# Kernel tuning notes

Hardware: AMD Instinct MI355X
Metric: run time of the kernel (lower is better)

## Reference

```python
import jax, jax.numpy as jnp
import numpy as np

N = 100000
C_IN = 128
HEADS = 4
D_HEAD = 32
E = 1600000
NEG_SLOPE = 0.2
LN_EPS = 1e-5


def setup_inputs() -> dict:
    key = jax.random.key(0)
    ks = jax.random.split(key, 8)
    x = jax.random.normal(ks[0], (N, C_IN), dtype=jnp.float32)
    edge_index = jax.random.randint(ks[1], (2, E), 0, N, dtype=jnp.int32)
    # LayerNorm affine params
    ln_gamma = jnp.ones((C_IN,), jnp.float32)
    ln_beta = jnp.zeros((C_IN,), jnp.float32)
    # GATv2 linear layers (lin_l for source/messages, lin_r for target), glorot-ish scale
    scale = 1.0 / np.sqrt(C_IN)
    W_l = jax.random.normal(ks[2], (C_IN, HEADS * D_HEAD), jnp.float32) * scale
    b_l = jnp.zeros((HEADS * D_HEAD,), jnp.float32)
    W_r = jax.random.normal(ks[3], (C_IN, HEADS * D_HEAD), jnp.float32) * scale
    b_r = jnp.zeros((HEADS * D_HEAD,), jnp.float32)
    att = jax.random.normal(ks[4], (HEADS, D_HEAD), jnp.float32) * (1.0 / np.sqrt(D_HEAD))
    bias = jnp.zeros((D_HEAD,), jnp.float32)  # concat=False -> out_channels bias
    return {"x": x, "edge_index": edge_index, "ln_gamma": ln_gamma, "ln_beta": ln_beta,
            "W_l": W_l, "b_l": b_l, "W_r": W_r, "b_r": b_r, "att": att, "bias": bias}


def reference(x, edge_index, ln_gamma, ln_beta, W_l, b_l, W_r, b_r, att, bias):
    n = x.shape[0]
    # LayerNorm + ReLU (dropout_mask=None / eval mode)
    mu = jnp.mean(x, axis=-1, keepdims=True)
    var = jnp.mean(jnp.square(x - mu), axis=-1, keepdims=True)
    xh = (x - mu) * jax.lax.rsqrt(var + LN_EPS) * ln_gamma + ln_beta
    xh = jax.nn.relu(xh)
    # add self loops
    loops = jnp.arange(n, dtype=edge_index.dtype)
    src = jnp.concatenate([edge_index[0], loops])  # message sources j
    dst = jnp.concatenate([edge_index[1], loops])  # aggregation targets i
    # GATv2: separate transforms for source and target
    x_l = (xh @ W_l + b_l).reshape(n, HEADS, D_HEAD)
    x_r = (xh @ W_r + b_r).reshape(n, HEADS, D_HEAD)
    # edge scores: e_ij = att . leaky_relu(x_l[j] + x_r[i])
    s = x_l[src] + x_r[dst]                                      # [E+N, H, Dh]
    e = jnp.einsum('ehd,hd->eh', jax.nn.leaky_relu(s, NEG_SLOPE), att)
    # segment softmax over destination node
    m = jax.ops.segment_max(e, dst, num_segments=n)              # [N, H]
    w = jnp.exp(e - m[dst])
    denom = jax.ops.segment_sum(w, dst, num_segments=n)          # [N, H]
    alpha = w / (denom[dst] + 1e-16)                             # [E+N, H]
    # scatter-aggregate messages alpha * x_l[j]
    out = jax.ops.segment_sum(alpha[:, :, None] * x_l[src], dst, num_segments=n)  # [N, H, Dh]
    # concat=False -> mean over heads, then bias
    return out.mean(axis=1) + bias
```

## Files before the change

kernel.cpp:

```cpp
#include <hip/hip_runtime.h>
#include <math.h>


typedef __bf16 bf16x8 __attribute__((ext_vector_type(8)));
typedef float f32x4 __attribute__((ext_vector_type(4)));
typedef _Float16 h2 __attribute__((ext_vector_type(2)));

#define BIN_T 4096
#define NB_MAX 1024
#define AST 136
#define HST 136

static __device__ __forceinline__ unsigned short f2bf(float f) {
  union { float f; unsigned u; } v;
  v.f = f;
  const unsigned r = v.u + 0x7fffu + ((v.u >> 16) & 1u);
  return (unsigned short)(r >> 16);
}
static __device__ __forceinline__ float bf2f(unsigned short h) {
  union { float f; unsigned u; } v;
  v.u = ((unsigned)h) << 16;
  return v.f;
}

static __device__ __forceinline__ float quad_reduce_add(float p) {
  int a = __builtin_amdgcn_mov_dpp(__builtin_bit_cast(int, p),
                                   0xB1 , 0xf, 0xf,
                                   true);
  p += __builtin_bit_cast(float, a);
  int b = __builtin_amdgcn_mov_dpp(__builtin_bit_cast(int, p),
                                   0x4E , 0xf, 0xf,
                                   true);
  p += __builtin_bit_cast(float, b);
  return p;
}

__global__ __launch_bounds__(256) void pack_w_k(
    const float* __restrict__ Wl, const float* __restrict__ Wr,
    unsigned short* __restrict__ wph, unsigned short* __restrict__ wpl) {
  const int idx = blockIdx.x * 256 + threadIdx.x;
  const int mat = idx >> 14;
  const int rem = idx & 16383;
  const int k = rem >> 7;
  const int c = rem & 127;
  const float v = (mat ? Wr : Wl)[rem];
  const unsigned short h = f2bf(v);
  const unsigned short lo = f2bf(v - bf2f(h));
  const int po = ((mat * 4 + (k >> 5)) * 128 + c) * 32 + (k & 31);
  wph[po] = h;
  wpl[po] = lo;
}

__global__ __launch_bounds__(512, 5) void ln_gemm_mfma_k(
    const float* __restrict__ x, const float* __restrict__ gamma,
    const float* __restrict__ beta,
    const unsigned short* __restrict__ wph,
    const unsigned short* __restrict__ wpl,
    const float* __restrict__ bl, const float* __restrict__ br,
    _Float16* __restrict__ xl16, _Float16* __restrict__ xr16, int n) {
  __shared__ char smem[64 * AST * 2 * 2];
  unsigned short* const ah = (unsigned short*)smem;
  unsigned short* const al = ah + 64 * AST;
  _Float16* const sth = (_Float16*)smem;

  const int t = threadIdx.x;
  const int blk = blockIdx.x * 64;

  {
    const int r = t >> 3, q = t & 7;
    const int node = blk + r;
    float4 v[4];
    float s = 0.f, s2 = 0.f;
    const float* xrow = x + (size_t)node * 128;
#pragma unroll
    for (int rep = 0; rep < 4; rep++) {
      float4 f = make_float4(0.f, 0.f, 0.f, 0.f);
      if (node < n) f = *(const float4*)(xrow + 4 * q + 32 * rep);
      v[rep] = f;
      s += f.x + f.y + f.z + f.w;
      s2 += f.x * f.x + f.y * f.y + f.z * f.z + f.w * f.w;
    }
    s += __shfl_xor(s, 1);  s += __shfl_xor(s, 2);  s += __shfl_xor(s, 4);
    s2 += __shfl_xor(s2, 1); s2 += __shfl_xor(s2, 2); s2 += __shfl_xor(s2, 4);
    const float mu = s * (1.f / 128.f);
    const float rs = rsqrtf(s2 * (1.f / 128.f) - mu * mu + 1e-5f);
#pragma unroll
    for (int rep = 0; rep < 4; rep++) {
      const int k0 = 4 * q + 32 * rep;
      const float4 g4 = *(const float4*)(gamma + k0);
      const float4 b4 = *(const float4*)(beta + k0);
      const float ev[4] = {v[rep].x, v[rep].y, v[rep].z, v[rep].w};
      const float gv[4] = {g4.x, g4.y, g4.z, g4.w};
      const float bv[4] = {b4.x, b4.y, b4.z, b4.w};
      unsigned short hs[4], ls[4];
#pragma unroll
      for (int i2 = 0; i2 < 4; i2++) {
        float xv = (ev[i2] - mu) * rs * gv[i2] + bv[i2];
        xv = fmaxf(xv, 0.f);
        const unsigned short h = f2bf(xv);
        hs[i2] = h;
        ls[i2] = f2bf(xv - bf2f(h));
      }
      *(ushort4*)(&ah[r * AST + k0]) = make_ushort4(hs[0], hs[1], hs[2], hs[3]);
      *(ushort4*)(&al[r * AST + k0]) = make_ushort4(ls[0], ls[1], ls[2], ls[3]);
    }
  }
  __syncthreads();

  const int lane = t & 63;
  const int w = t >> 6;
  const int mat = w >> 2;
  const int cbase = (w & 3) * 32;
  const int m16 = lane & 15;
  const int quad = lane >> 4;
  const float* const biasp = mat ? br : bl;

  f32x4 acc[2][4];
  float bc[2];
#pragma unroll
  for (int ct = 0; ct < 2; ct++) {
    const int c = cbase + ct * 16 + m16;
    bf16x8 Bh[4], Bl8[4];
#pragma unroll
    for (int kb = 0; kb < 4; kb++) {
      const int bo = ((mat * 4 + kb) * 128 + c) * 32 + quad * 8;
      Bh[kb]  = *(const bf16x8*)(wph + bo);
      Bl8[kb] = *(const bf16x8*)(wpl + bo);
    }
    bc[ct] = biasp[c];
#pragma unroll
    for (int rt = 0; rt < 4; rt++) {
      f32x4 a = {0.f, 0.f, 0.f, 0.f};
#pragma unroll
      for (int kb = 0; kb < 4; kb++) {
        const int ao = (rt * 16 + m16) * AST + kb * 32 + quad * 8;
        const bf16x8 Ah  = *(const bf16x8*)(ah + ao);
        const bf16x8 Al8 = *(const bf16x8*)(al + ao);
        a = __builtin_amdgcn_mfma_f32_16x16x32_bf16(Ah,  Bh[kb],  a, 0, 0, 0);
        a = __builtin_amdgcn_mfma_f32_16x16x32_bf16(Al8, Bh[kb],  a, 0, 0, 0);
        a = __builtin_amdgcn_mfma_f32_16x16x32_bf16(Ah,  Bl8[kb], a, 0, 0, 0);
      }
      acc[ct][rt] = a;
    }
  }

  unsigned short* const outs[2] = {(unsigned short*)xl16,
                                   (unsigned short*)xr16};
#pragma unroll
  for (int round = 0; round < 2; round++) {
    __syncthreads();
    if (mat == 1 - round) {
#pragma unroll
      for (int ct = 0; ct < 2; ct++)
#pragma unroll
        for (int rt = 0; rt < 4; rt++)
#pragma unroll
          for (int g = 0; g < 4; g++)
            sth[(rt * 16 + quad * 4 + g) * HST + cbase + ct * 16 + m16] =
                (_Float16)(acc[ct][rt][g] + bc[ct]);
    }
    __syncthreads();
    unsigned short* const dst = outs[1 - round];
#pragma unroll
    for (int pass = 0; pass < 2; pass++) {
      const int idx = pass * 512 + t;
      const int row = idx >> 4;
      const int c8 = (idx & 15) * 8;
      const int node = blk + row;
      if (node < n)
        *(uint4*)(dst + (size_t)node * 128 + c8) =
            *(const uint4*)((const unsigned short*)sth + row * HST + c8);
    }
  }
}

__global__ __launch_bounds__(256) void hist_lds_k(
    const int* __restrict__ dst_arr, int* __restrict__ bucket_cnt,
    int E, int NB) {
  __shared__ int h[NB_MAX];
  const int t = threadIdx.x;
  for (int b = t; b < NB; b += 256) h[b] = 0;
  __syncthreads();
  const int beg = blockIdx.x * BIN_T;
  const int end = min(beg + BIN_T, E);
  for (int j0 = beg + t * 4; j0 < end; j0 += 1024) {
    if (j0 + 4 <= end) {
      const int4 d4 = *(const int4*)(dst_arr + j0);
      atomicAdd(&h[d4.x >> 7], 1);
      atomicAdd(&h[d4.y >> 7], 1);
      atomicAdd(&h[d4.z >> 7], 1);
      atomicAdd(&h[d4.w >> 7], 1);
    } else {
      for (int j = j0; j < end; j++) atomicAdd(&h[dst_arr[j] >> 7], 1);
    }
  }
  __syncthreads();
  for (int b = t; b < NB; b += 256) {
    const int v = h[b];
    if (v) atomicAdd(&bucket_cnt[b], v);
  }
}

__global__ __launch_bounds__(1024) void bucket_scan_k(
    const int* __restrict__ bucket_cnt, int* __restrict__ bucket_edge_off,
    int* __restrict__ bucket_cur, int* __restrict__ offsets,
    int NB, int N, int M) {
  __shared__ int lds[1024];
  const int t = threadIdx.x;
  const int v = (t < NB) ? bucket_cnt[t] : 0;
  lds[t] = v;
  __syncthreads();
  for (int d = 1; d < 1024; d <<= 1) {
    int u = 0;
    if (t >= d) u = lds[t - d];
    __syncthreads();
    lds[t] += u;
    __syncthreads();
  }
  if (t < NB) {
    const int excl = lds[t] - v;
    bucket_edge_off[t] = excl;
    bucket_cur[t] = excl;
    if (t == NB - 1) bucket_edge_off[NB] = lds[t];
  }
  if (t == 0) offsets[N] = M;
}

__global__ __launch_bounds__(256) void bin2_k(
    const int* __restrict__ ei, int* __restrict__ bucket_cur,
    unsigned* __restrict__ binned, int E, int NB) {
  __shared__ int h[NB_MAX];
  __shared__ int cur[NB_MAX];
  const int t = threadIdx.x;
  for (int b = t; b < NB; b += 256) h[b] = 0;
  __syncthreads();
  const int beg = blockIdx.x * BIN_T;
  const int end = min(beg + BIN_T, E);
  for (int j0 = beg + t * 4; j0 < end; j0 += 1024) {
    if (j0 + 4 <= end) {
      const int4 d4 = *(const int4*)(ei + E + j0);
      atomicAdd(&h[d4.x >> 7], 1);
      atomicAdd(&h[d4.y >> 7], 1);
      atomicAdd(&h[d4.z >> 7], 1);
      atomicAdd(&h[d4.w >> 7], 1);
    } else {
      for (int j = j0; j < end; j++) atomicAdd(&h[ei[E + j] >> 7], 1);
    }
  }
  __syncthreads();
  for (int b = t; b < NB; b += 256) {
    const int v = h[b];
    cur[b] = v ? atomicAdd(&bucket_cur[b], v) : 0;
  }
  __syncthreads();
  for (int j0 = beg + t * 4; j0 < end; j0 += 1024) {
    if (j0 + 4 <= end) {
      const int4 s4 = *(const int4*)(ei + j0);
      const int4 d4 = *(const int4*)(ei + E + j0);
      binned[atomicAdd(&cur[d4.x >> 7], 1)] =
          (((unsigned)d4.x & 127u) << 25) | (unsigned)s4.x;
      binned[atomicAdd(&cur[d4.y >> 7], 1)] =
          (((unsigned)d4.y & 127u) << 25) | (unsigned)s4.y;
      binned[atomicAdd(&cur[d4.z >> 7], 1)] =
          (((unsigned)d4.z & 127u) << 25) | (unsigned)s4.z;
      binned[atomicAdd(&cur[d4.w >> 7], 1)] =
          (((unsigned)d4.w & 127u) << 25) | (unsigned)s4.w;
    } else {
      for (int j = j0; j < end; j++) {
        const int s = ei[j], d = ei[E + j];
        binned[atomicAdd(&cur[d >> 7], 1)] =
            (((unsigned)d & 127u) << 25) | (unsigned)s;
      }
    }
  }
}

__global__ __launch_bounds__(256) void csr_build_k(
    const unsigned* __restrict__ binned,
    const int* __restrict__ bucket_edge_off,
    unsigned* __restrict__ csr_src, int* __restrict__ offsets, int N, int M) {
  __shared__ int s_cnt[128];
  __shared__ int s_off[128];
  __shared__ int s_cur[128];
  const int b = blockIdx.x;
  const int t = threadIdx.x;
  if (b == 0 && t < 16) csr_src[M + t] = 0;
  const int eb = bucket_edge_off[b];
  const int ee = bucket_edge_off[b + 1];
  const int node0 = b << 7;
  if (t < 128) s_cnt[t] = 0;
  __syncthreads();
  for (int j = eb + t; j < ee; j += 256) {
    atomicAdd(&s_cnt[binned[j] >> 25], 1);
  }
  __syncthreads();
  int w = 0;
  if (t < 128) w = (node0 + t < N) ? (s_cnt[t] + 1) : 0;
  if (t < 128) s_off[t] = w;
  __syncthreads();
  for (int d = 1; d < 128; d <<= 1) {
    int u = 0;
    if (t < 128 && t >= d) u = s_off[t - d];
    __syncthreads();
    if (t < 128) s_off[t] += u;
    __syncthreads();
  }
  const int base = eb + node0;
  if (t < 128) {
    const int excl = s_off[t] - w;
    const int node = node0 + t;
    if (node < N) {
      offsets[node] = base + excl;
      csr_src[base + excl] = (unsigned)node << 8;
      s_cur[t] = excl + 1;
    }
  }
  __syncthreads();
  for (int j = eb + t; j < ee; j += 256) {
    const unsigned e = binned[j];
    const int pos = atomicAdd(&s_cur[e >> 25], 1);
    csr_src[base + pos] = (e & 0x1ffffffu) << 8;
  }
}

__global__ __launch_bounds__(256) void agg_fused_k(
    const uint4* __restrict__ xl4, const uint4* __restrict__ xr4,
    const float* __restrict__ att, const unsigned* __restrict__ csr_src,
    const int* __restrict__ offsets, const float* __restrict__ bias,
    float* __restrict__ out, int n) {
  const int t = threadIdx.x;
  const int wid = t >> 6;
  const int lane = t & 63;
  const int u = lane & 15;
  const int g = lane >> 4;
  const int nwaves = gridDim.x * 4;

  h2 at[4];
  {
    const float L2E = 1.44269504f;
    const float4 a0 = *(const float4*)(att + u * 8);
    const float4 a1 = *(const float4*)(att + u * 8 + 4);
    at[0] = h2{(_Float16)(a0.x * L2E), (_Float16)(a0.y * L2E)};
    at[1] = h2{(_Float16)(a0.z * L2E), (_Float16)(a0.w * L2E)};
    at[2] = h2{(_Float16)(a1.x * L2E), (_Float16)(a1.y * L2E)};
    at[3] = h2{(_Float16)(a1.z * L2E), (_Float16)(a1.w * L2E)};
  }
  float4 b0, b1;
  if (lane < 4) {
    b0 = *(const float4*)(bias + lane * 8);
    b1 = *(const float4*)(bias + lane * 8 + 4);
  }

  const h2 slope = h2{(_Float16)0.2f, (_Float16)0.2f};
  const char* const xbu = (const char*)xl4 + ((unsigned)u << 4);
  union U { uint4 u4; h2 h[4]; unsigned ui[4]; };

  int i = blockIdx.x * 4 + wid;
  if (i >= n) return;

  int off = offsets[i];
  int end = offsets[i + 1];
  U xru; xru.u4 = xr4[(size_t)i * 16 + u];
  uint4 rA = *(const uint4*)(xbu + csr_src[off + g]);
  uint4 rB = *(const uint4*)(xbu + csr_src[off + 4 + g]);

  while (true) {
    const int inext = i + nwaves;
    const int isel = (inext < n) ? inext : i;
    const int offn = offsets[isel];
    const int endn = offsets[isel + 1];
    U xrn; xrn.u4 = xr4[(size_t)isel * 16 + u];

    float den = 0.f;
    float acc[8] = {0.f, 0.f, 0.f, 0.f, 0.f, 0.f, 0.f, 0.f};

    for (int jb = off; jb < end; jb += 4) {
      U xv; xv.u4 = rA;
      rA = rB;
      rB = *(const uint4*)(xbu + csr_src[jb + 8 + g]);

      float p = 0.f;
#pragma unroll
      for (int k = 0; k < 4; k++) {
        const h2 s = xv.h[k] + xru.h[k];
        const h2 l = __builtin_elementwise_max(s, s * slope);
        p = __builtin_amdgcn_fdot2(l, at[k], p, false);
      }
      p = quad_reduce_add(p);

      const float wgt = (jb + g < end) ? __builtin_amdgcn_exp2f(p) : 0.f;
      den += wgt;
#pragma unroll
      for (int k = 0; k < 4; k++) {
        asm("v_fma_mix_f32 %0, %1, %2, %0 op_sel:[0,0,0] op_sel_hi:[0,1,0]"
            : "+v"(acc[2 * k]) : "v"(wgt), "v"(xv.ui[k]));
        asm("v_fma_mix_f32 %0, %1, %2, %0 op_sel:[0,1,0] op_sel_hi:[0,1,0]"
            : "+v"(acc[2 * k + 1]) : "v"(wgt), "v"(xv.ui[k]));
      }
    }

    const unsigned niA = csr_src[offn + g];
    const unsigned niB = csr_src[offn + 4 + g];

    den += __shfl_xor(den, 16);
    den += __shfl_xor(den, 32);
#pragma unroll
    for (int m = 0; m < 8; m++) {
      acc[m] += __shfl_xor(acc[m], 16);
      acc[m] += __shfl_xor(acc[m], 32);
    }
    const float rd = 1.0f / (den + 1e-16f);
#pragma unroll
    for (int m = 0; m < 8; m++) acc[m] *= rd;
#pragma unroll
    for (int m = 0; m < 8; m++) {
      acc[m] += __shfl_xor(acc[m], 4);
      acc[m] += __shfl_xor(acc[m], 8);
    }
    if (lane < 4) {
      float4 o0 = make_float4(acc[0] * 0.25f + b0.x, acc[1] * 0.25f + b0.y,
                              acc[2] * 0.25f + b0.z, acc[3] * 0.25f + b0.w);
      float4 o1 = make_float4(acc[4] * 0.25f + b1.x, acc[5] * 0.25f + b1.y,
                              acc[6] * 0.25f + b1.z, acc[7] * 0.25f + b1.w);
      *(float4*)(out + (size_t)i * 32 + lane * 8) = o0;
      *(float4*)(out + (size_t)i * 32 + lane * 8 + 4) = o1;
    }

    if (inext >= n) break;
    i = inext;
    off = offn;
    end = endn;
    xru = xrn;
    rA = *(const uint4*)(xbu + niA);
    rB = *(const uint4*)(xbu + niB);
  }
}

extern "C" void kernel_launch(void* const* d_in, const int* in_sizes, int n_in,
                              void* d_out, int out_size, void* d_ws,
                              size_t ws_size, hipStream_t stream) {
  const float* x     = (const float*)d_in[0];
  const int*   ei    = (const int*)d_in[1];
  const float* gamma = (const float*)d_in[2];
  const float* beta  = (const float*)d_in[3];
  const float* Wl    = (const float*)d_in[4];
  const float* bl    = (const float*)d_in[5];
  const float* Wr    = (const float*)d_in[6];
  const float* br    = (const float*)d_in[7];
  const float* att   = (const float*)d_in[8];
  const float* bias  = (const float*)d_in[9];
  float* out = (float*)d_out;

  const int N = in_sizes[0] / 128;
  const int E = in_sizes[1] / 2;
  const int M = E + N;
  const int NB = (N + 127) / 128;
  const int nchunks = (E + BIN_T - 1) / BIN_T;

  char* p = (char*)d_ws;
  size_t o = 0;
  auto alloc = [&](size_t bytes) -> void* {
    void* r = (void*)(p + o);
    o = (o + bytes + 255) & ~(size_t)255;
    return r;
  };
  _Float16* xl16   = (_Float16*)alloc((size_t)N * 128 * 2);
  unsigned* binned = (unsigned*)xl16;
  _Float16* xr16 = (_Float16*)alloc((size_t)N * 128 * 2);
  unsigned* csr_src = (unsigned*)alloc((size_t)M * 4 + 64);
  int*   offsets = (int*)alloc((size_t)(N + 1) * 4);
  int*   bucket_cnt = (int*)alloc((size_t)NB * 4);
  int*   bucket_off = (int*)alloc((size_t)(NB + 1) * 4);
  int*   bucket_cur = (int*)alloc((size_t)NB * 4);
  unsigned short* wph = (unsigned short*)alloc(2 * 128 * 128 * 2);
  unsigned short* wpl = (unsigned short*)alloc(2 * 128 * 128 * 2);
  (void)n_in; (void)out_size; (void)ws_size;

  hipMemsetAsync(bucket_cnt, 0, (size_t)NB * 4, stream);
  hist_lds_k<<<nchunks, 256, 0, stream>>>(ei + E, bucket_cnt, E, NB);
  bucket_scan_k<<<1, 1024, 0, stream>>>(bucket_cnt, bucket_off, bucket_cur,
                                        offsets, NB, N, M);
  bin2_k<<<nchunks, 256, 0, stream>>>(ei, bucket_cur, binned, E, NB);
  csr_build_k<<<NB, 256, 0, stream>>>(binned, bucket_off, csr_src, offsets,
                                      N, M);

  pack_w_k<<<128, 256, 0, stream>>>(Wl, Wr, wph, wpl);
  ln_gemm_mfma_k<<<(N + 63) / 64, 512, 0, stream>>>(x, gamma, beta, wph, wpl,
                                                    bl, br, xl16, xr16, N);

  const int nodeWaves = (N + 3) / 4;
  const int aggBlocks = nodeWaves < 2048 ? nodeWaves : 2048;
  agg_fused_k<<<aggBlocks, 256, 0, stream>>>((const uint4*)xl16,
                                             (const uint4*)xr16, att,
                                             csr_src, offsets, bias, out, N);
}
```

Before: 257.6 us.

## Fold bucket scan and weight packing into neighboring kernels to cut launches

Removes the separate bucket_scan and pack_w kernels. The weight bf16 split-packing moves into the histogram kernel, and each bin2/csr_build block recomputes the bucket prefix scan from the raw counts. bin2 now starts from a zeroed per-bucket cursor plus the scanned offset. BIN_T is doubled, which halves the block count for histogram and binning. Two fewer launches and their serialization gaps are traded for a redundant scan in every block and fewer, larger binning blocks.

```diff
diff --git a/kernel.cpp b/kernel.cpp
--- a/kernel.cpp
+++ b/kernel.cpp
@@ -6,7 +6,7 @@
 typedef float f32x4 __attribute__((ext_vector_type(4)));
 typedef _Float16 h2 __attribute__((ext_vector_type(2)));
 
-#define BIN_T 4096
+#define BIN_T 8192
 #define NB_MAX 1024
 #define AST 136
 #define HST 136
@@ -33,22 +33,6 @@
                                    true);
   p += __builtin_bit_cast(float, b);
   return p;
-}
-
-__global__ __launch_bounds__(256) void pack_w_k(
-    const float* __restrict__ Wl, const float* __restrict__ Wr,
-    unsigned short* __restrict__ wph, unsigned short* __restrict__ wpl) {
-  const int idx = blockIdx.x * 256 + threadIdx.x;
-  const int mat = idx >> 14;
-  const int rem = idx & 16383;
-  const int k = rem >> 7;
-  const int c = rem & 127;
-  const float v = (mat ? Wr : Wl)[rem];
-  const unsigned short h = f2bf(v);
-  const unsigned short lo = f2bf(v - bf2f(h));
-  const int po = ((mat * 4 + (k >> 5)) * 128 + c) * 32 + (k & 31);
-  wph[po] = h;
-  wpl[po] = lo;
 }
 
 __global__ __launch_bounds__(512, 5) void ln_gemm_mfma_k(
@@ -174,12 +158,27 @@
   }
 }
 
-__global__ __launch_bounds__(256) void hist_lds_k(
+__global__ __launch_bounds__(256) void hist_pack_k(
     const int* __restrict__ dst_arr, int* __restrict__ bucket_cnt,
+    const float* __restrict__ Wl, const float* __restrict__ Wr,
+    unsigned short* __restrict__ wph, unsigned short* __restrict__ wpl,
     int E, int NB) {
   __shared__ int h[NB_MAX];
   const int t = threadIdx.x;
+  const int gtid = blockIdx.x * 256 + t;
   for (int b = t; b < NB; b += 256) h[b] = 0;
+  if (gtid < 32768) {
+    const int mat = gtid >> 14;
+    const int rem = gtid & 16383;
+    const int k = rem >> 7;
+    const int c = rem & 127;
+    const float v = (mat ? Wr : Wl)[rem];
+    const unsigned short hh = f2bf(v);
+    const unsigned short lo = f2bf(v - bf2f(hh));
+    const int po = ((mat * 4 + (k >> 5)) * 128 + c) * 32 + (k & 31);
+    wph[po] = hh;
+    wpl[po] = lo;
+  }
   __syncthreads();
   const int beg = blockIdx.x * BIN_T;
   const int end = min(beg + BIN_T, E);
@@ -201,36 +200,13 @@
   }
 }
 
-__global__ __launch_bounds__(1024) void bucket_scan_k(
-    const int* __restrict__ bucket_cnt, int* __restrict__ bucket_edge_off,
-    int* __restrict__ bucket_cur, int* __restrict__ offsets,
-    int NB, int N, int M) {
-  __shared__ int lds[1024];
-  const int t = threadIdx.x;
-  const int v = (t < NB) ? bucket_cnt[t] : 0;
-  lds[t] = v;
-  __syncthreads();
-  for (int d = 1; d < 1024; d <<= 1) {
-    int u = 0;
-    if (t >= d) u = lds[t - d];
-    __syncthreads();
-    lds[t] += u;
-    __syncthreads();
-  }
-  if (t < NB) {
-    const int excl = lds[t] - v;
-    bucket_edge_off[t] = excl;
-    bucket_cur[t] = excl;
-    if (t == NB - 1) bucket_edge_off[NB] = lds[t];
-  }
-  if (t == 0) offsets[N] = M;
-}
-
 __global__ __launch_bounds__(256) void bin2_k(
-    const int* __restrict__ ei, int* __restrict__ bucket_cur,
-    unsigned* __restrict__ binned, int E, int NB) {
+    const int* __restrict__ ei, const int* __restrict__ bucket_cnt,
+    int* __restrict__ bucket_cur, unsigned* __restrict__ binned,
+    int E, int NB) {
   __shared__ int h[NB_MAX];
   __shared__ int cur[NB_MAX];
+  __shared__ int ld2[256];
   const int t = threadIdx.x;
   for (int b = t; b < NB; b += 256) h[b] = 0;
   __syncthreads();
@@ -248,9 +224,32 @@
     }
   }
   __syncthreads();
-  for (int b = t; b < NB; b += 256) {
-    const int v = h[b];
-    cur[b] = v ? atomicAdd(&bucket_cur[b], v) : 0;
+  {
+    int pre[4], gsum = 0;
+#pragma unroll
+    for (int k = 0; k < 4; k++) {
+      const int idx = t * 4 + k;
+      const int v = (idx < NB) ? bucket_cnt[idx] : 0;
+      pre[k] = gsum;
+      gsum += v;
+    }
+    ld2[t] = gsum;
+    __syncthreads();
+    for (int d = 1; d < 256; d <<= 1) {
+      int uv = (t >= d) ? ld2[t - d] : 0;
+      __syncthreads();
+      ld2[t] += uv;
+      __syncthreads();
+    }
+    const int ex = (t > 0) ? ld2[t - 1] : 0;
+#pragma unroll
+    for (int k = 0; k < 4; k++) {
+      const int idx = t * 4 + k;
+      if (idx < NB) {
+        const int v = h[idx];
+        cur[idx] = ex + pre[k] + (v ? atomicAdd(&bucket_cur[idx], v) : 0);
+      }
+    }
   }
   __syncthreads();
   for (int j0 = beg + t * 4; j0 < end; j0 += 1024) {
@@ -276,20 +275,47 @@
 }
 
 __global__ __launch_bounds__(256) void csr_build_k(
-    const unsigned* __restrict__ binned,
-    const int* __restrict__ bucket_edge_off,
-    unsigned* __restrict__ csr_src, int* __restrict__ offsets, int N, int M) {
+    const unsigned* __restrict__ binned, const int* __restrict__ bucket_cnt,
+    unsigned* __restrict__ csr_src, int* __restrict__ offsets,
+    int N, int M, int NB) {
   __shared__ int s_cnt[128];
   __shared__ int s_off[128];
   __shared__ int s_cur[128];
+  __shared__ int ld2[256];
+  __shared__ int s_eb;
   const int b = blockIdx.x;
   const int t = threadIdx.x;
   if (b == 0 && t < 16) csr_src[M + t] = 0;
-  const int eb = bucket_edge_off[b];
-  const int ee = bucket_edge_off[b + 1];
+  if (b == 0 && t == 0) offsets[N] = M;
+  {
+    int pre[4], gsum = 0;
+#pragma unroll
+    for (int k = 0; k < 4; k++) {
+      const int idx = t * 4 + k;
+      const int v = (idx < NB) ? bucket_cnt[idx] : 0;
+      pre[k] = gsum;
+      gsum += v;
+    }
+    ld2[t] = gsum;
+    __syncthreads();
+    for (int d = 1; d < 256; d <<= 1) {
+      int uv = (t >= d) ? ld2[t - d] : 0;
+      __syncthreads();
+      ld2[t] += uv;
+      __syncthreads();
+    }
+    const int ex = (t > 0) ? ld2[t - 1] : 0;
+#pragma unroll
+    for (int k = 0; k < 4; k++) {
+      const int idx = t * 4 + k;
+      if (idx == b) s_eb = ex + pre[k];
+    }
+  }
+  if (t < 128) s_cnt[t] = 0;
+  __syncthreads();
+  const int eb = s_eb;
+  const int ee = eb + bucket_cnt[b];
   const int node0 = b << 7;
-  if (t < 128) s_cnt[t] = 0;
-  __syncthreads();
   for (int j = eb + t; j < ee; j += 256) {
     atomicAdd(&s_cnt[binned[j] >> 25], 1);
   }
@@ -469,22 +495,23 @@
   _Float16* xr16 = (_Float16*)alloc((size_t)N * 128 * 2);
   unsigned* csr_src = (unsigned*)alloc((size_t)M * 4 + 64);
   int*   offsets = (int*)alloc((size_t)(N + 1) * 4);
-  int*   bucket_cnt = (int*)alloc((size_t)NB * 4);
-  int*   bucket_off = (int*)alloc((size_t)(NB + 1) * 4);
-  int*   bucket_cur = (int*)alloc((size_t)NB * 4);
+  int*   bucket_cnt = (int*)alloc((size_t)NB * 2 * 4);
+  int*   bucket_cur = bucket_cnt + NB;
   unsigned short* wph = (unsigned short*)alloc(2 * 128 * 128 * 2);
   unsigned short* wpl = (unsigned short*)alloc(2 * 128 * 128 * 2);
   (void)n_in; (void)out_size; (void)ws_size;
 
-  hipMemsetAsync(bucket_cnt, 0, (size_t)NB * 4, stream);
-  hist_lds_k<<<nchunks, 256, 0, stream>>>(ei + E, bucket_cnt, E, NB);
-  bucket_scan_k<<<1, 1024, 0, stream>>>(bucket_cnt, bucket_off, bucket_cur,
-                                        offsets, NB, N, M);
-  bin2_k<<<nchunks, 256, 0, stream>>>(ei, bucket_cur, binned, E, NB);
-  csr_build_k<<<NB, 256, 0, stream>>>(binned, bucket_off, csr_src, offsets,
-                                      N, M);
-
-  pack_w_k<<<128, 256, 0, stream>>>(Wl, Wr, wph, wpl);
+  hipMemsetAsync(bucket_cnt, 0, (size_t)NB * 2 * 4, stream);
+  {
+    const int grid = nchunks > 128 ? nchunks : 128;
+    hist_pack_k<<<grid, 256, 0, stream>>>(ei + E, bucket_cnt, Wl, Wr, wph,
+                                          wpl, E, NB);
+  }
+  bin2_k<<<nchunks, 256, 0, stream>>>(ei, bucket_cnt, bucket_cur, binned,
+                                      E, NB);
+  csr_build_k<<<NB, 256, 0, stream>>>(binned, bucket_cnt, csr_src, offsets,
+                                      N, M, NB);
+
   ln_gemm_mfma_k<<<(N + 63) / 64, 512, 0, stream>>>(x, gamma, beta, wph, wpl,
                                                     bl, br, xl16, xr16, N);
 
```

Result: slower. 269.2 us (+4.5%).

## Merge weight packing into histogram and co-schedule binning with LN-GEMM blocks

Applied to the files above, without the earlier changes.

Folds the weight bf16 hi/lo packing into the histogram kernel, so the first edge-index pass also does the packing. The edge binning pass and the LayerNorm+MFMA GEMM now run in one launch, with the first nchunks blocks binning edges and the rest computing xl/xr. Because xl16 is now written at the same time as binning, the binned scratch moves into the output buffer, which csr_build consumes before the aggregation kernel overwrites it. This removes two launches and lets the memory-bound scatter overlap the compute-heavy GEMM. In exchange the binning blocks now run with 512 threads, capped by the GEMM's launch bounds.

```diff
diff --git a/kernel.cpp b/kernel.cpp
--- a/kernel.cpp
+++ b/kernel.cpp
@@ -35,151 +35,27 @@
   return p;
 }
 
-__global__ __launch_bounds__(256) void pack_w_k(
+__global__ __launch_bounds__(256) void hist_pack_k(
+    const int* __restrict__ dst_arr, int* __restrict__ bucket_cnt,
     const float* __restrict__ Wl, const float* __restrict__ Wr,
-    unsigned short* __restrict__ wph, unsigned short* __restrict__ wpl) {
-  const int idx = blockIdx.x * 256 + threadIdx.x;
-  const int mat = idx >> 14;
-  const int rem = idx & 16383;
-  const int k = rem >> 7;
-  const int c = rem & 127;
-  const float v = (mat ? Wr : Wl)[rem];
-  const unsigned short h = f2bf(v);
-  const unsigned short lo = f2bf(v - bf2f(h));
-  const int po = ((mat * 4 + (k >> 5)) * 128 + c) * 32 + (k & 31);
-  wph[po] = h;
-  wpl[po] = lo;
-}
-
-__global__ __launch_bounds__(512, 5) void ln_gemm_mfma_k(
-    const float* __restrict__ x, const float* __restrict__ gamma,
-    const float* __restrict__ beta,
-    const unsigned short* __restrict__ wph,
-    const unsigned short* __restrict__ wpl,
-    const float* __restrict__ bl, const float* __restrict__ br,
-    _Float16* __restrict__ xl16, _Float16* __restrict__ xr16, int n) {
-  __shared__ char smem[64 * AST * 2 * 2];
-  unsigned short* const ah = (unsigned short*)smem;
-  unsigned short* const al = ah + 64 * AST;
-  _Float16* const sth = (_Float16*)smem;
-
-  const int t = threadIdx.x;
-  const int blk = blockIdx.x * 64;
-
-  {
-    const int r = t >> 3, q = t & 7;
-    const int node = blk + r;
-    float4 v[4];
-    float s = 0.f, s2 = 0.f;
-    const float* xrow = x + (size_t)node * 128;
-#pragma unroll
-    for (int rep = 0; rep < 4; rep++) {
-      float4 f = make_float4(0.f, 0.f, 0.f, 0.f);
-      if (node < n) f = *(const float4*)(xrow + 4 * q + 32 * rep);
-      v[rep] = f;
-      s += f.x + f.y + f.z + f.w;
-      s2 += f.x * f.x + f.y * f.y + f.z * f.z + f.w * f.w;
-    }
-    s += __shfl_xor(s, 1);  s += __shfl_xor(s, 2);  s += __shfl_xor(s, 4);
-    s2 += __shfl_xor(s2, 1); s2 += __shfl_xor(s2, 2); s2 += __shfl_xor(s2, 4);
-    const float mu = s * (1.f / 128.f);
-    const float rs = rsqrtf(s2 * (1.f / 128.f) - mu * mu + 1e-5f);
-#pragma unroll
-    for (int rep = 0; rep < 4; rep++) {
-      const int k0 = 4 * q + 32 * rep;
-      const float4 g4 = *(const float4*)(gamma + k0);
-      const float4 b4 = *(const float4*)(beta + k0);
-      const float ev[4] = {v[rep].x, v[rep].y, v[rep].z, v[rep].w};
-      const float gv[4] = {g4.x, g4.y, g4.z, g4.w};
-      const float bv[4] = {b4.x, b4.y, b4.z, b4.w};
-      unsigned short hs[4], ls[4];
-#pragma unroll
-      for (int i2 = 0; i2 < 4; i2++) {
-        float xv = (ev[i2] - mu) * rs * gv[i2] + bv[i2];
-        xv = fmaxf(xv, 0.f);
-        const unsigned short h = f2bf(xv);
-        hs[i2] = h;
-        ls[i2] = f2bf(xv - bf2f(h));
-      }
-      *(ushort4*)(&ah[r * AST + k0]) = make_ushort4(hs[0], hs[1], hs[2], hs[3]);
-      *(ushort4*)(&al[r * AST + k0]) = make_ushort4(ls[0], ls[1], ls[2], ls[3]);
-    }
-  }
-  __syncthreads();
-
-  const int lane = t & 63;
-  const int w = t >> 6;
-  const int mat = w >> 2;
-  const int cbase = (w & 3) * 32;
-  const int m16 = lane & 15;
-  const int quad = lane >> 4;
-  const float* const biasp = mat ? br : bl;
-
-  f32x4 acc[2][4];
-  float bc[2];
-#pragma unroll
-  for (int ct = 0; ct < 2; ct++) {
-    const int c = cbase + ct * 16 + m16;
-    bf16x8 Bh[4], Bl8[4];
-#pragma unroll
-    for (int kb = 0; kb < 4; kb++) {
-      const int bo = ((mat * 4 + kb) * 128 + c) * 32 + quad * 8;
-      Bh[kb]  = *(const bf16x8*)(wph + bo);
-      Bl8[kb] = *(const bf16x8*)(wpl + bo);
-    }
-    bc[ct] = biasp[c];
-#pragma unroll
-    for (int rt = 0; rt < 4; rt++) {
-      f32x4 a = {0.f, 0.f, 0.f, 0.f};
-#pragma unroll
-      for (int kb = 0; kb < 4; kb++) {
-        const int ao = (rt * 16 + m16) * AST + kb * 32 + quad * 8;
-        const bf16x8 Ah  = *(const bf16x8*)(ah + ao);
-        const bf16x8 Al8 = *(const bf16x8*)(al + ao);
-        a = __builtin_amdgcn_mfma_f32_16x16x32_bf16(Ah,  Bh[kb],  a, 0, 0, 0);
-        a = __builtin_amdgcn_mfma_f32_16x16x32_bf16(Al8, Bh[kb],  a, 0, 0, 0);
-        a = __builtin_amdgcn_mfma_f32_16x16x32_bf16(Ah,  Bl8[kb], a, 0, 0, 0);
-      }
-      acc[ct][rt] = a;
-    }
-  }
-
-  unsigned short* const outs[2] = {(unsigned short*)xl16,
-                                   (unsigned short*)xr16};
-#pragma unroll
-  for (int round = 0; round < 2; round++) {
-    __syncthreads();
-    if (mat == 1 - round) {
-#pragma unroll
-      for (int ct = 0; ct < 2; ct++)
-#pragma unroll
-        for (int rt = 0; rt < 4; rt++)
-#pragma unroll
-          for (int g = 0; g < 4; g++)
-            sth[(rt * 16 + quad * 4 + g) * HST + cbase + ct * 16 + m16] =
-                (_Float16)(acc[ct][rt][g] + bc[ct]);
-    }
-    __syncthreads();
-    unsigned short* const dst = outs[1 - round];
-#pragma unroll
-    for (int pass = 0; pass < 2; pass++) {
-      const int idx = pass * 512 + t;
-      const int row = idx >> 4;
-      const int c8 = (idx & 15) * 8;
-      const int node = blk + row;
-      if (node < n)
-        *(uint4*)(dst + (size_t)node * 128 + c8) =
-            *(const uint4*)((const unsigned short*)sth + row * HST + c8);
-    }
-  }
-}
-
-__global__ __launch_bounds__(256) void hist_lds_k(
-    const int* __restrict__ dst_arr, int* __restrict__ bucket_cnt,
+    unsigned short* __restrict__ wph, unsigned short* __restrict__ wpl,
     int E, int NB) {
   __shared__ int h[NB_MAX];
   const int t = threadIdx.x;
+  const int gtid = blockIdx.x * 256 + t;
   for (int b = t; b < NB; b += 256) h[b] = 0;
+  if (gtid < 32768) {
+    const int mat = gtid >> 14;
+    const int rem = gtid & 16383;
+    const int k = rem >> 7;
+    const int c = rem & 127;
+    const float v = (mat ? Wr : Wl)[rem];
+    const unsigned short hh = f2bf(v);
+    const unsigned short lo = f2bf(v - bf2f(hh));
+    const int po = ((mat * 4 + (k >> 5)) * 128 + c) * 32 + (k & 31);
+    wph[po] = hh;
+    wpl[po] = lo;
+  }
   __syncthreads();
   const int beg = blockIdx.x * BIN_T;
   const int end = min(beg + BIN_T, E);
@@ -226,51 +102,175 @@
   if (t == 0) offsets[N] = M;
 }
 
-__global__ __launch_bounds__(256) void bin2_k(
+__global__ __launch_bounds__(512, 5) void gemm_bin_fat_k(
+    const float* __restrict__ x, const float* __restrict__ gamma,
+    const float* __restrict__ beta,
+    const unsigned short* __restrict__ wph,
+    const unsigned short* __restrict__ wpl,
+    const float* __restrict__ bl, const float* __restrict__ br,
+    _Float16* __restrict__ xl16, _Float16* __restrict__ xr16,
     const int* __restrict__ ei, int* __restrict__ bucket_cur,
-    unsigned* __restrict__ binned, int E, int NB) {
-  __shared__ int h[NB_MAX];
-  __shared__ int cur[NB_MAX];
+    unsigned* __restrict__ binned,
+    int n, int E, int NB, int nchunks) {
+  __shared__ char smem[64 * AST * 2 * 2];
   const int t = threadIdx.x;
-  for (int b = t; b < NB; b += 256) h[b] = 0;
-  __syncthreads();
-  const int beg = blockIdx.x * BIN_T;
-  const int end = min(beg + BIN_T, E);
-  for (int j0 = beg + t * 4; j0 < end; j0 += 1024) {
-    if (j0 + 4 <= end) {
-      const int4 d4 = *(const int4*)(ei + E + j0);
-      atomicAdd(&h[d4.x >> 7], 1);
-      atomicAdd(&h[d4.y >> 7], 1);
-      atomicAdd(&h[d4.z >> 7], 1);
-      atomicAdd(&h[d4.w >> 7], 1);
-    } else {
-      for (int j = j0; j < end; j++) atomicAdd(&h[ei[E + j] >> 7], 1);
-    }
-  }
-  __syncthreads();
-  for (int b = t; b < NB; b += 256) {
-    const int v = h[b];
-    cur[b] = v ? atomicAdd(&bucket_cur[b], v) : 0;
-  }
-  __syncthreads();
-  for (int j0 = beg + t * 4; j0 < end; j0 += 1024) {
-    if (j0 + 4 <= end) {
-      const int4 s4 = *(const int4*)(ei + j0);
-      const int4 d4 = *(const int4*)(ei + E + j0);
-      binned[atomicAdd(&cur[d4.x >> 7], 1)] =
-          (((unsigned)d4.x & 127u) << 25) | (unsigned)s4.x;
-      binned[atomicAdd(&cur[d4.y >> 7], 1)] =
-          (((unsigned)d4.y & 127u) << 25) | (unsigned)s4.y;
-      binned[atomicAdd(&cur[d4.z >> 7], 1)] =
-          (((unsigned)d4.z & 127u) << 25) | (unsigned)s4.z;
-      binned[atomicAdd(&cur[d4.w >> 7], 1)] =
-          (((unsigned)d4.w & 127u) << 25) | (unsigned)s4.w;
-    } else {
-      for (int j = j0; j < end; j++) {
-        const int s = ei[j], d = ei[E + j];
-        binned[atomicAdd(&cur[d >> 7], 1)] =
-            (((unsigned)d & 127u) << 25) | (unsigned)s;
+
+  if ((int)blockIdx.x < nchunks) {
+    int* const h = (int*)smem;
+    int* const cur = h + NB_MAX;
+    for (int b = t; b < NB; b += 512) h[b] = 0;
+    __syncthreads();
+    const int beg = blockIdx.x * BIN_T;
+    const int end = min(beg + BIN_T, E);
+    for (int j0 = beg + t * 4; j0 < end; j0 += 2048) {
+      if (j0 + 4 <= end) {
+        const int4 d4 = *(const int4*)(ei + E + j0);
+        atomicAdd(&h[d4.x >> 7], 1);
+        atomicAdd(&h[d4.y >> 7], 1);
+        atomicAdd(&h[d4.z >> 7], 1);
+        atomicAdd(&h[d4.w >> 7], 1);
+      } else {
+        for (int j = j0; j < end; j++) atomicAdd(&h[ei[E + j] >> 7], 1);
       }
+    }
+    __syncthreads();
+    for (int b = t; b < NB; b += 512) {
+      const int v = h[b];
+      cur[b] = v ? atomicAdd(&bucket_cur[b], v) : 0;
+    }
+    __syncthreads();
+    for (int j0 = beg + t * 4; j0 < end; j0 += 2048) {
+      if (j0 + 4 <= end) {
+        const int4 s4 = *(const int4*)(ei + j0);
+        const int4 d4 = *(const int4*)(ei + E + j0);
+        binned[atomicAdd(&cur[d4.x >> 7], 1)] =
+            (((unsigned)d4.x & 127u) << 25) | (unsigned)s4.x;
+        binned[atomicAdd(&cur[d4.y >> 7], 1)] =
+            (((unsigned)d4.y & 127u) << 25) | (unsigned)s4.y;
+        binned[atomicAdd(&cur[d4.z >> 7], 1)] =
+            (((unsigned)d4.z & 127u) << 25) | (unsigned)s4.z;
+        binned[atomicAdd(&cur[d4.w >> 7], 1)] =
+            (((unsigned)d4.w & 127u) << 25) | (unsigned)s4.w;
+      } else {
+        for (int j = j0; j < end; j++) {
+          const int s = ei[j], d = ei[E + j];
+          binned[atomicAdd(&cur[d >> 7], 1)] =
+              (((unsigned)d & 127u) << 25) | (unsigned)s;
+        }
+      }
+    }
+    return;
+  }
+
+  unsigned short* const ah = (unsigned short*)smem;
+  unsigned short* const al = ah + 64 * AST;
+  _Float16* const sth = (_Float16*)smem;
+  const int blk = (blockIdx.x - nchunks) * 64;
+
+  {
+    const int r = t >> 3, q = t & 7;
+    const int node = blk + r;
+    float4 v[4];
+    float s = 0.f, s2 = 0.f;
+    const float* xrow = x + (size_t)node * 128;
+#pragma unroll
+    for (int rep = 0; rep < 4; rep++) {
+      float4 f = make_float4(0.f, 0.f, 0.f, 0.f);
+      if (node < n) f = *(const float4*)(xrow + 4 * q + 32 * rep);
+      v[rep] = f;
+      s += f.x + f.y + f.z + f.w;
+      s2 += f.x * f.x + f.y * f.y + f.z * f.z + f.w * f.w;
+    }
+    s += __shfl_xor(s, 1);  s += __shfl_xor(s, 2);  s += __shfl_xor(s, 4);
+    s2 += __shfl_xor(s2, 1); s2 += __shfl_xor(s2, 2); s2 += __shfl_xor(s2, 4);
+    const float mu = s * (1.f / 128.f);
+    const float rs = rsqrtf(s2 * (1.f / 128.f) - mu * mu + 1e-5f);
+#pragma unroll
+    for (int rep = 0; rep < 4; rep++) {
+      const int k0 = 4 * q + 32 * rep;
+      const float4 g4 = *(const float4*)(gamma + k0);
+      const float4 b4 = *(const float4*)(beta + k0);
+      const float ev[4] = {v[rep].x, v[rep].y, v[rep].z, v[rep].w};
+      const float gv[4] = {g4.x, g4.y, g4.z, g4.w};
+      const float bv[4] = {b4.x, b4.y, b4.z, b4.w};
+      unsigned short hs[4], ls[4];
+#pragma unroll
+      for (int i2 = 0; i2 < 4; i2++) {
+        float xv = (ev[i2] - mu) * rs * gv[i2] + bv[i2];
+        xv = fmaxf(xv, 0.f);
+        const unsigned short h = f2bf(xv);
+        hs[i2] = h;
+        ls[i2] = f2bf(xv - bf2f(h));
+      }
+      *(ushort4*)(&ah[r * AST + k0]) = make_ushort4(hs[0], hs[1], hs[2], hs[3]);
+      *(ushort4*)(&al[r * AST + k0]) = make_ushort4(ls[0], ls[1], ls[2], ls[3]);
+    }
+  }
+  __syncthreads();
+
+  const int lane = t & 63;
+  const int w = t >> 6;
+  const int mat = w >> 2;
+  const int cbase = (w & 3) * 32;
+  const int m16 = lane & 15;
+  const int quad = lane >> 4;
+  const float* const biasp = mat ? br : bl;
+
+  f32x4 acc[2][4];
+  float bc[2];
+#pragma unroll
+  for (int ct = 0; ct < 2; ct++) {
+    const int c = cbase + ct * 16 + m16;
+    bf16x8 Bh[4], Bl8[4];
+#pragma unroll
+    for (int kb = 0; kb < 4; kb++) {
+      const int bo = ((mat * 4 + kb) * 128 + c) * 32 + quad * 8;
+      Bh[kb]  = *(const bf16x8*)(wph + bo);
+      Bl8[kb] = *(const bf16x8*)(wpl + bo);
+    }
+    bc[ct] = biasp[c];
+#pragma unroll
+    for (int rt = 0; rt < 4; rt++) {
+      f32x4 a = {0.f, 0.f, 0.f, 0.f};
+#pragma unroll
+      for (int kb = 0; kb < 4; kb++) {
+        const int ao = (rt * 16 + m16) * AST + kb * 32 + quad * 8;
+        const bf16x8 Ah  = *(const bf16x8*)(ah + ao);
+        const bf16x8 Al8 = *(const bf16x8*)(al + ao);
+        a = __builtin_amdgcn_mfma_f32_16x16x32_bf16(Ah,  Bh[kb],  a, 0, 0, 0);
+        a = __builtin_amdgcn_mfma_f32_16x16x32_bf16(Al8, Bh[kb],  a, 0, 0, 0);
+        a = __builtin_amdgcn_mfma_f32_16x16x32_bf16(Ah,  Bl8[kb], a, 0, 0, 0);
+      }
+      acc[ct][rt] = a;
+    }
+  }
+
+  unsigned short* const outs[2] = {(unsigned short*)xl16,
+                                   (unsigned short*)xr16};
+#pragma unroll
+  for (int round = 0; round < 2; round++) {
+    __syncthreads();
+    if (mat == 1 - round) {
+#pragma unroll
+      for (int ct = 0; ct < 2; ct++)
+#pragma unroll
+        for (int rt = 0; rt < 4; rt++)
+#pragma unroll
+          for (int g = 0; g < 4; g++)
+            sth[(rt * 16 + quad * 4 + g) * HST + cbase + ct * 16 + m16] =
+                (_Float16)(acc[ct][rt][g] + bc[ct]);
+    }
+    __syncthreads();
+    unsigned short* const dst = outs[1 - round];
+#pragma unroll
+    for (int pass = 0; pass < 2; pass++) {
+      const int idx = pass * 512 + t;
+      const int row = idx >> 4;
+      const int c8 = (idx & 15) * 8;
+      const int node = blk + row;
+      if (node < n)
+        *(uint4*)(dst + (size_t)node * 128 + c8) =
+            *(const uint4*)((const unsigned short*)sth + row * HST + c8);
     }
   }
 }
@@ -464,8 +464,7 @@
     o = (o + bytes + 255) & ~(size_t)255;
     return r;
   };
-  _Float16* xl16   = (_Float16*)alloc((size_t)N * 128 * 2);
-  unsigned* binned = (unsigned*)xl16;
+  _Float16* xl16 = (_Float16*)alloc((size_t)N * 128 * 2);
   _Float16* xr16 = (_Float16*)alloc((size_t)N * 128 * 2);
   unsigned* csr_src = (unsigned*)alloc((size_t)M * 4 + 64);
   int*   offsets = (int*)alloc((size_t)(N + 1) * 4);
@@ -474,19 +473,24 @@
   int*   bucket_cur = (int*)alloc((size_t)NB * 4);
   unsigned short* wph = (unsigned short*)alloc(2 * 128 * 128 * 2);
   unsigned short* wpl = (unsigned short*)alloc(2 * 128 * 128 * 2);
+  unsigned* binned = (unsigned*)out;
   (void)n_in; (void)out_size; (void)ws_size;
 
   hipMemsetAsync(bucket_cnt, 0, (size_t)NB * 4, stream);
-  hist_lds_k<<<nchunks, 256, 0, stream>>>(ei + E, bucket_cnt, E, NB);
+  hist_pack_k<<<nchunks, 256, 0, stream>>>(ei + E, bucket_cnt, Wl, Wr, wph,
+                                           wpl, E, NB);
   bucket_scan_k<<<1, 1024, 0, stream>>>(bucket_cnt, bucket_off, bucket_cur,
                                         offsets, NB, N, M);
-  bin2_k<<<nchunks, 256, 0, stream>>>(ei, bucket_cur, binned, E, NB);
+
+  {
+    const int gemmBlocks = (N + 63) / 64;
+    gemm_bin_fat_k<<<nchunks + gemmBlocks, 512, 0, stream>>>(
+        x, gamma, beta, wph, wpl, bl, br, xl16, xr16,
+        ei, bucket_cur, binned, N, E, NB, nchunks);
+  }
+
   csr_build_k<<<NB, 256, 0, stream>>>(binned, bucket_off, csr_src, offsets,
                                       N, M);
-
-  pack_w_k<<<128, 256, 0, stream>>>(Wl, Wr, wph, wpl);
-  ln_gemm_mfma_k<<<(N + 63) / 64, 512, 0, stream>>>(x, gamma, beta, wph, wpl,
-                                                    bl, br, xl16, xr16, N);
 
   const int nodeWaves = (N + 3) / 4;
   const int aggBlocks = nodeWaves < 2048 ? nodeWaves : 2048;
```

Result: faster. 246.1 us (-4.4%).
